# Performance work log

Hardware: AMD Instinct MI355X
Metric: run time of the kernel (lower is better)

The kernel has to match this reference:

```python
import jax, jax.numpy as jnp
import numpy as np

B, T = 16, 64
IN, H = 256, 512          # input_size, hidden_size (= output_size)
M, W, R = 256, 64, 4      # nr_cells, cell_size, read_heads
NN_IN = R * W + IN        # controller input size = 512
IFACE = R * W + 3 * W + 5 * R + 3  # 471
DELTA = 1e-6


def _lin(key, fan_out, fan_in):
    k1, k2 = jax.random.split(key)
    s = 1.0 / np.sqrt(fan_in)
    Wm = jax.random.uniform(k1, (fan_out, fan_in), minval=-s, maxval=s, dtype=jnp.float32)
    b = jax.random.uniform(k2, (fan_out,), minval=-s, maxval=s, dtype=jnp.float32)
    return Wm, b


def setup_inputs() -> dict:
    key = jax.random.key(0)
    ks = jax.random.split(key, 8)
    x = jax.random.normal(ks[0], (B, T, IN), dtype=jnp.float32)
    Wih0, bih0 = _lin(ks[1], 4 * H, NN_IN)
    Whh0, bhh0 = _lin(ks[2], 4 * H, H)
    Wih1, bih1 = _lin(ks[3], 4 * H, H)
    Whh1, bhh1 = _lin(ks[4], 4 * H, H)
    Wout, bout = _lin(ks[5], H, H)              # output_weights
    Wif, bif = _lin(ks[6], IFACE, H)            # memory interface_weights
    Wmem, bmem = _lin(ks[7], IN, R * W + H)     # mem_out
    return dict(x=x, Wih0=Wih0, bih0=bih0, Whh0=Whh0, bhh0=bhh0,
                Wih1=Wih1, bih1=bih1, Whh1=Whh1, bhh1=bhh1,
                Wout=Wout, bout=bout, Wif=Wif, bif=bif, Wmem=Wmem, bmem=bmem)


def _lstm(x, h, c, Wih, bih, Whh, bhh):
    g = x @ Wih.T + bih + h @ Whh.T + bhh
    i, f, gg, o = jnp.split(g, 4, axis=-1)  # torch LSTMCell gate order i,f,g,o
    i, f, o = jax.nn.sigmoid(i), jax.nn.sigmoid(f), jax.nn.sigmoid(o)
    c = f * c + i * jnp.tanh(gg)
    return o * jnp.tanh(c), c


def _content_weights(mem, keys, strengths):
    # mem (B,M,W), keys (B,K,W), strengths (B,K) -> softmax cosine weights (B,K,M)
    mn = mem / (jnp.linalg.norm(mem, axis=2, keepdims=True) + DELTA)
    kn = keys / (jnp.linalg.norm(keys, axis=2, keepdims=True) + DELTA)
    sim = jnp.einsum('bkw,bmw->bkm', kn, mn)
    return jax.nn.softmax(sim * strengths[:, :, None], axis=2)


def _dnc_forward(x, Wih0, bih0, Whh0, bhh0, Wih1, bih1, Whh1, bhh1,
                 Wout, bout, Wif, bif, Wmem, bmem):
    Bz, Tz = x.shape[0], x.shape[1]
    eye_mask = 1.0 - jnp.eye(M, dtype=x.dtype)
    # NOTE: in the source, last_read (zeros at init) is concatenated to EVERY
    # timestep's input and never updated inside the layer time loop.
    last_read = jnp.zeros((Bz, Tz, R * W), dtype=x.dtype)
    xs = jnp.swapaxes(jnp.concatenate([x, last_read], axis=-1), 0, 1)  # (T,B,NN_IN)

    def step(carry, xt):
        h0, c0, h1, c1, mem, link, prec, rw, ww, usage = carry
        h0, c0 = _lstm(xt, h0, c0, Wih0, bih0, Whh0, bhh0)
        h1, c1 = _lstm(h0, h1, c1, Wih1, bih1, Whh1, bhh1)
        out = h1 @ Wout.T + bout
        xi = h1 @ Wif.T + bif  # (B, IFACE)
        o1 = R * W
        rk = jnp.tanh(xi[:, :o1]).reshape(Bz, R, W)
        rs = jax.nn.softplus(xi[:, o1:o1 + R])
        o2 = o1 + R
        wk = jnp.tanh(xi[:, o2:o2 + W]).reshape(Bz, 1, W)
        ws = jax.nn.softplus(xi[:, o2 + W:o2 + W + 1])          # (B,1)
        ev = jax.nn.sigmoid(xi[:, o2 + W + 1:o2 + 2 * W + 1])   # erase (B,W)
        wv = jnp.tanh(xi[:, o2 + 2 * W + 1:o2 + 3 * W + 1])     # write vec (B,W)
        o3 = o2 + 3 * W + 1
        fg = jax.nn.sigmoid(xi[:, o3:o3 + R])                   # free gates (B,R)
        ag = jax.nn.sigmoid(xi[:, o3 + R:o3 + R + 1])           # alloc gate (B,1)
        wg = jax.nn.sigmoid(xi[:, o3 + R + 1:o3 + R + 2])       # write gate (B,1)
        rm = jax.nn.softmax(xi[:, o3 + R + 2:].reshape(Bz, R, 3), axis=-1)
        # --- usage update (single write head: 1 - prod(1-ww) == ww) ---
        usage = usage + (1.0 - usage) * ww
        psi = jnp.prod(1.0 - fg[:, :, None] * rw, axis=1)
        usage = usage * psi
        # --- write content weighting ---
        wcw = _content_weights(mem, wk, ws)[:, 0]  # (B,M)
        # --- allocation via sort + exclusive cumprod + inverse scatter ---
        u = DELTA + (1.0 - DELTA) * usage
        idx = jnp.argsort(u, axis=1)  # ascending usage = free list
        su = jnp.take_along_axis(u, idx, axis=1)
        prod_excl = jnp.cumprod(jnp.concatenate([jnp.ones((Bz, 1), u.dtype), su], 1), axis=1)[:, :-1]
        sa = (1.0 - su) * prod_excl
        alloc = jnp.take_along_axis(sa, jnp.argsort(idx, axis=1), axis=1)  # (B,M)
        # --- write weighting ---
        ww = wg * (ag * alloc + (1.0 - ag) * wcw)  # (B,M)
        # --- memory erase + write ---
        mem = mem * (1.0 - ww[:, :, None] * ev[:, None, :]) + ww[:, :, None] * wv[:, None, :]
        # --- temporal link matrix (diag zeroed) + precedence ---
        link = (1.0 - ww[:, :, None] - ww[:, None, :]) * link + ww[:, :, None] * prec[:, None, :]
        link = link * eye_mask
        prec = (1.0 - jnp.sum(ww, axis=1, keepdims=True)) * prec + ww
        # --- read: content + forward/backward directional modes ---
        cw = _content_weights(mem, rk, rs)            # (B,R,M)
        fwd = jnp.einsum('bmn,brn->brm', link, rw)    # L @ rw_prev
        bwd = jnp.einsum('brm,bmn->brn', rw, link)    # rw_prev @ L
        rw = rm[:, :, 0:1] * bwd + rm[:, :, 1:2] * fwd + rm[:, :, 2:3] * cw
        read_vecs = jnp.einsum('brm,bmw->brw', rw, mem).reshape(Bz, R * W)
        y = jnp.concatenate([out, read_vecs], axis=1) @ Wmem.T + bmem  # mem_out, dropout=0
        return (h0, c0, h1, c1, mem, link, prec, rw, ww, usage), y

    z = lambda *s: jnp.zeros(s, dtype=x.dtype)
    init = (z(Bz, H), z(Bz, H), z(Bz, H), z(Bz, H),
            z(Bz, M, W), z(Bz, M, M), z(Bz, M), z(Bz, R, M), z(Bz, M), z(Bz, M))
    _, ys = jax.lax.scan(step, init, xs)
    return jnp.swapaxes(ys, 0, 1)  # (B,T,IN)


def reference(x, Wih0, bih0, Whh0, bhh0, Wih1, bih1, Whh1, bhh1,
              Wout, bout, Wif, bif, Wmem, bmem):
    return _dnc_forward(x, Wih0, bih0, Whh0, bhh0, Wih1, bih1, Whh1, bhh1,
                        Wout, bout, Wif, bif, Wmem, bmem)
```

## Files before the change

### kernel.cpp

```cpp
#include <hip/hip_runtime.h>
#include <math.h>


#define BZ    16
#define TZ    64
#define HID   512
#define NCELL 256
#define CSZ   64
#define NRD   4
#define G4H   2048
#define IFC   471
#define DEL   1e-6f
#define SMT   257

__device__ __forceinline__ float sig_(float x) { return 1.f / (1.f + expf(-x)); }
__device__ __forceinline__ float splus_(float x) { return fmaxf(x, 0.f) + log1pf(expf(-fabsf(x))); }

__global__ __launch_bounds__(256) void k_transpose(const float* __restrict__ src,
                                                   float* __restrict__ dst,
                                                   int rows, int cols, int kmax, int dst_stride) {
  __shared__ float tile[32][33];
  int c0 = blockIdx.x * 32, r0 = blockIdx.y * 32;
  int tx = threadIdx.x, ty = threadIdx.y;
  for (int i = ty; i < 32; i += 8) {
    int r = r0 + i, c = c0 + tx;
    tile[i][tx] = (r < rows && c < cols) ? src[(size_t)r * cols + c] : 0.f;
  }
  __syncthreads();
  for (int i = ty; i < 32; i += 8) {
    int c = c0 + i, r = r0 + tx;
    if (c < kmax && r < rows) dst[(size_t)c * dst_stride + r] = tile[tx][i];
  }
}

__global__ __launch_bounds__(256) void k_xpart(const float* __restrict__ x,
                                               const float* __restrict__ Wih0T,
                                               const float* __restrict__ bih0,
                                               const float* __restrict__ bhh0,
                                               float* __restrict__ xpart) {
  const int lane = threadIdx.x, ty = threadIdx.y;
  const int jg = blockIdx.x * 64 + lane;
  const int tb0 = blockIdx.y * 16;
  __shared__ float sx[16][256];
  const int tid = ty * 64 + lane;
  for (int idx = tid; idx < 16 * 256; idx += 256) {
    int row = idx >> 8, k = idx & 255;
    int tb = tb0 + row, tt = tb >> 4, bb = tb & 15;
    sx[row][k] = x[((size_t)bb * TZ + tt) * 256 + k];
  }
  __syncthreads();
  float acc[4] = {0.f, 0.f, 0.f, 0.f};
  for (int k = 0; k < 256; ++k) {
    float wv = Wih0T[(size_t)k * G4H + jg];
#pragma unroll
    for (int i = 0; i < 4; ++i) acc[i] = fmaf(wv, sx[ty * 4 + i][k], acc[i]);
  }
  float bias = bih0[jg] + bhh0[jg];
#pragma unroll
  for (int i = 0; i < 4; ++i)
    xpart[(size_t)(tb0 + ty * 4 + i) * G4H + jg] = acc[i] + bias;
}

__global__ __launch_bounds__(256) void k_lstm_step(
    const float* __restrict__ xpart,
    const float* __restrict__ Whh0T,
    const float* __restrict__ Wih1T, const float* __restrict__ Whh1T,
    const float* __restrict__ bih1, const float* __restrict__ bhh1,
    float* __restrict__ h0, float* __restrict__ c0,
    float* __restrict__ h1, float* __restrict__ c1,
    float* __restrict__ h1_all, int ph) {
  const int jl = threadIdx.x, ks = threadIdx.y;
  const int tid = ks * 64 + jl;
  const int bid = blockIdx.x;
  const int grp = bid >> 7;
  const int lb = bid & 127;
  const int b = lb >> 3, jb = lb & 7;
  const int j = jb * 64 + jl;
  __shared__ float sh0[512], sh1[512];
  __shared__ float sred[4][4][64];

  if (grp == 0) {
    if (ph >= TZ) return;
    const int t = ph, po = t & 1, pn = po ^ 1;
    const float* h0o = h0 + ((size_t)po * BZ + b) * HID;
    for (int k = tid; k < 512; k += 256) sh0[k] = h0o[k];
    __syncthreads();
    float a0 = 0.f, a1 = 0.f, a2 = 0.f, a3 = 0.f;
    const int kb = ks * 128;
#pragma unroll 8
    for (int k = kb; k < kb + 128; ++k) {
      const float hk = sh0[k];
      const float* wr = Whh0T + (size_t)k * G4H + j;
      a0 = fmaf(hk, wr[0], a0);
      a1 = fmaf(hk, wr[512], a1);
      a2 = fmaf(hk, wr[1024], a2);
      a3 = fmaf(hk, wr[1536], a3);
    }
    sred[ks][0][jl] = a0; sred[ks][1][jl] = a1; sred[ks][2][jl] = a2; sred[ks][3][jl] = a3;
    __syncthreads();
    if (ks == 0) {
      const float* xp = xpart + ((size_t)t * BZ + b) * G4H;
      float gi = sred[0][0][jl] + sred[1][0][jl] + sred[2][0][jl] + sred[3][0][jl] + xp[j];
      float gf = sred[0][1][jl] + sred[1][1][jl] + sred[2][1][jl] + sred[3][1][jl] + xp[512 + j];
      float gg = sred[0][2][jl] + sred[1][2][jl] + sred[2][2][jl] + sred[3][2][jl] + xp[1024 + j];
      float go_ = sred[0][3][jl] + sred[1][3][jl] + sred[2][3][jl] + sred[3][3][jl] + xp[1536 + j];
      gi = sig_(gi); gf = sig_(gf); go_ = sig_(go_); gg = tanhf(gg);
      float* cp = c0 + b * HID + j;
      float cc = gf * (*cp) + gi * gg;
      *cp = cc;
      h0[((size_t)pn * BZ + b) * HID + j] = go_ * tanhf(cc);
    }
  } else {
    if (ph < 1) return;
    const int t = ph - 1, po = t & 1, pn = po ^ 1;
    const float* h0n = h0 + ((size_t)pn * BZ + b) * HID;
    const float* h1o = h1 + ((size_t)po * BZ + b) * HID;
    for (int k = tid; k < 512; k += 256) { sh0[k] = h0n[k]; sh1[k] = h1o[k]; }
    __syncthreads();
    float a0 = 0.f, a1 = 0.f, a2 = 0.f, a3 = 0.f;
    const int kb = ks * 128;
#pragma unroll 4
    for (int k = kb; k < kb + 128; ++k) {
      const float x0 = sh0[k], x1 = sh1[k];
      const float* wi = Wih1T + (size_t)k * G4H + j;
      const float* wh = Whh1T + (size_t)k * G4H + j;
      a0 = fmaf(x0, wi[0], fmaf(x1, wh[0], a0));
      a1 = fmaf(x0, wi[512], fmaf(x1, wh[512], a1));
      a2 = fmaf(x0, wi[1024], fmaf(x1, wh[1024], a2));
      a3 = fmaf(x0, wi[1536], fmaf(x1, wh[1536], a3));
    }
    sred[ks][0][jl] = a0; sred[ks][1][jl] = a1; sred[ks][2][jl] = a2; sred[ks][3][jl] = a3;
    __syncthreads();
    if (ks == 0) {
      float gi = sred[0][0][jl] + sred[1][0][jl] + sred[2][0][jl] + sred[3][0][jl] + bih1[j] + bhh1[j];
      float gf = sred[0][1][jl] + sred[1][1][jl] + sred[2][1][jl] + sred[3][1][jl] + bih1[512 + j] + bhh1[512 + j];
      float gg = sred[0][2][jl] + sred[1][2][jl] + sred[2][2][jl] + sred[3][2][jl] + bih1[1024 + j] + bhh1[1024 + j];
      float go_ = sred[0][3][jl] + sred[1][3][jl] + sred[2][3][jl] + sred[3][3][jl] + bih1[1536 + j] + bhh1[1536 + j];
      gi = sig_(gi); gf = sig_(gf); go_ = sig_(go_); gg = tanhf(gg);
      float* cp = c1 + b * HID + j;
      float cc = gf * (*cp) + gi * gg;
      *cp = cc;
      float hv = go_ * tanhf(cc);
      h1[((size_t)pn * BZ + b) * HID + j] = hv;
      h1_all[((size_t)t * BZ + b) * HID + j] = hv;
    }
  }
}

__global__ __launch_bounds__(256) void k_xiout(const float* __restrict__ h1_all,
                                               const float* __restrict__ WoutT,
                                               const float* __restrict__ WifT,
                                               const float* __restrict__ bout,
                                               const float* __restrict__ bif,
                                               float* __restrict__ out_all,
                                               float* __restrict__ xi_all) {
  const int lane = threadIdx.x, ty = threadIdx.y;
  const int u = blockIdx.x * 64 + lane;
  const int row0 = blockIdx.y * 16;
  __shared__ float sh[16][512];
  const int tid = ty * 64 + lane;
  for (int idx = tid; idx < 16 * 512; idx += 256) {
    int r2 = idx >> 9, k = idx & 511;
    sh[r2][k] = h1_all[(size_t)(row0 + r2) * 512 + k];
  }
  __syncthreads();
  const bool isout = (u < 512);
  int uc = isout ? u : (u - 512);
  if (!isout && uc >= IFC) uc = 0;
  const float* wcol = isout ? (WoutT + u) : (WifT + uc);
  float bias = isout ? bout[u] : ((u - 512) < IFC ? bif[u - 512] : 0.f);
  float acc[4] = {0.f, 0.f, 0.f, 0.f};
  for (int k = 0; k < 512; ++k) {
    float wv = wcol[(size_t)k * 512];
#pragma unroll
    for (int i = 0; i < 4; ++i) acc[i] = fmaf(wv, sh[ty * 4 + i][k], acc[i]);
  }
#pragma unroll
  for (int i = 0; i < 4; ++i) {
    int row = row0 + ty * 4 + i;
    if (isout) out_all[(size_t)row * 512 + u] = acc[i] + bias;
    else if ((u - 512) < IFC) xi_all[(size_t)row * 512 + (u - 512)] = acc[i] + bias;
  }
}

__global__ __launch_bounds__(1024, 1) void k_memchain(const float* __restrict__ xi_all,
                                                      float* __restrict__ linkg,
                                                      float* __restrict__ rv_all) {
  const int b = blockIdx.x;
  const int tid = threadIdx.x;
  const int lane = tid & 63;
  const int wv = tid >> 6;
  const int m8 = tid & 255;
  const int seg = tid >> 8;
  float* LNK = linkg + (size_t)b * (NCELL * NCELL);

  __shared__ __align__(16) float smemT[CSZ * SMT];
  __shared__ __align__(16) float sxi[472];
  __shared__ __align__(16) float srkn[NRD][64];
  __shared__ __align__(16) float swkn[64];
  __shared__ __align__(16) float sev[64];
  __shared__ __align__(16) float swvv[64];
  __shared__ __align__(16) float sscal[40];
  __shared__ __align__(16) float srw[NRD][256];
  __shared__ __align__(16) float sww[256];
  __shared__ __align__(16) float susage[256];
  __shared__ __align__(16) float sprec[256];
  __shared__ __align__(16) float ssim[NRD][256];
  __shared__ __align__(16) float sfwd[NRD][256];
  __shared__ __align__(16) float sbwd[NRD][264];
  __shared__ __align__(16) float sa[256];
  __shared__ __align__(16) float sc_[256];
  __shared__ float sb_[256];
  __shared__ int srank[256];
  __shared__ __align__(16) float scr[4][5 * 264];
  __shared__ float sred2[64];

  for (int i = tid; i < CSZ * SMT; i += 1024) smemT[i] = 0.f;
  if (tid < 256) {
    sww[tid] = 0.f; susage[tid] = 0.f; sprec[tid] = 0.f;
    srw[0][tid] = 0.f; srw[1][tid] = 0.f; srw[2][tid] = 0.f; srw[3][tid] = 0.f;
  }
  for (int i = tid; i < (NCELL * NCELL) / 4; i += 1024)
    ((float4*)LNK)[i] = make_float4(0.f, 0.f, 0.f, 0.f);
  __syncthreads();

  for (int t = 0; t < TZ; ++t) {
    if (tid < IFC) sxi[tid] = xi_all[((size_t)t * BZ + b) * 512 + tid];
    __syncthreads();
    if (wv < 4) {
      float v = tanhf(sxi[wv * 64 + lane]);
      float s2 = v * v;
#pragma unroll
      for (int off = 32; off; off >>= 1) s2 += __shfl_xor(s2, off);
      srkn[wv][lane] = v / (sqrtf(s2) + DEL);
    } else if (wv == 4) {
      float v = tanhf(sxi[260 + lane]);
      float s2 = v * v;
#pragma unroll
      for (int off = 32; off; off >>= 1) s2 += __shfl_xor(s2, off);
      swkn[lane] = v / (sqrtf(s2) + DEL);
    } else if (wv == 5) {
      sev[lane] = sig_(sxi[325 + lane]);
    } else if (wv == 6) {
      swvv[lane] = tanhf(sxi[389 + lane]);
    } else if (wv == 7) {
      if (lane < 4) sscal[lane] = splus_(sxi[256 + lane]);
      if (lane == 4) sscal[4] = splus_(sxi[324]);
      if (lane >= 8 && lane < 12) sscal[lane] = sig_(sxi[453 + (lane - 8)]);
      if (lane == 12) sscal[12] = sig_(sxi[457]);
      if (lane == 13) sscal[13] = sig_(sxi[458]);
      if (lane >= 16 && lane < 20) {
        int r = lane - 16;
        float a = sxi[459 + r * 3], b2 = sxi[460 + r * 3], c2 = sxi[461 + r * 3];
        float mx3 = fmaxf(a, fmaxf(b2, c2));
        float ea = expf(a - mx3), eb = expf(b2 - mx3), ec = expf(c2 - mx3);
        float iv = 1.f / (ea + eb + ec);
        sscal[20 + r * 3 + 0] = ea * iv;
        sscal[20 + r * 3 + 1] = eb * iv;
        sscal[20 + r * 3 + 2] = ec * iv;
      }
    }
    __syncthreads();

    float un_r = 0.f;
    if (tid < 256) {
      float wwo = sww[tid], uo = susage[tid];
      float u1 = uo + (1.f - uo) * wwo;
      float psi = 1.f;
#pragma unroll
      for (int r = 0; r < 4; ++r) psi *= 1.f - sscal[8 + r] * srw[r][tid];
      un_r = u1 * psi;
      susage[tid] = un_r;
    }
    {
      float dot = 0.f, nn = 0.f;
#pragma unroll 4
      for (int w = seg * 16; w < seg * 16 + 16; ++w) {
        float mv = smemT[w * SMT + m8];
        dot = fmaf(mv, swkn[w], dot);
        nn = fmaf(mv, mv, nn);
      }
      scr[seg][0 * 264 + m8] = dot;
      scr[seg][1 * 264 + m8] = nn;
    }
    __syncthreads();
    float e_r = 0.f, simv = 0.f;
    if (tid < 256) {
      float dot = scr[0][tid] + scr[1][tid] + scr[2][tid] + scr[3][tid];
      float nn = scr[0][264 + tid] + scr[1][264 + tid] + scr[2][264 + tid] + scr[3][264 + tid];
      simv = sscal[4] * dot / (sqrtf(nn) + DEL);
      float mx = simv;
#pragma unroll
      for (int off = 32; off; off >>= 1) mx = fmaxf(mx, __shfl_xor(mx, off));
      if (lane == 0) sred2[wv] = mx;
    }
    __syncthreads();
    if (tid < 256) {
      float mx = fmaxf(fmaxf(sred2[0], sred2[1]), fmaxf(sred2[2], sred2[3]));
      e_r = expf(simv - mx);
      float s = e_r;
#pragma unroll
      for (int off = 32; off; off >>= 1) s += __shfl_xor(s, off);
      if (lane == 0) sred2[8 + wv] = s;
    }
    __syncthreads();
    float wcw_r = 0.f;
    if (tid < 256) {
      float sm = sred2[8] + sred2[9] + sred2[10] + sred2[11];
      wcw_r = e_r / sm;
      sa[tid] = DEL + (1.f - DEL) * un_r;
    }
    __syncthreads();

    {
      float um = sa[m8];
      int cnt = 0;
      for (int j2 = seg * 64; j2 < seg * 64 + 64; ++j2) {
        float uj = sa[j2];
        cnt += (uj < um || (uj == um && j2 < m8)) ? 1 : 0;
      }
      ((int*)scr[seg])[m8] = cnt;
    }
    __syncthreads();
    if (tid < 256) {
      int rank = ((int*)scr[0])[tid] + ((int*)scr[1])[tid] + ((int*)scr[2])[tid] + ((int*)scr[3])[tid];
      srank[tid] = rank;
      sb_[rank] = sa[tid];
    }
    __syncthreads();
    float inc = 0.f;
    if (tid < 256) {
      inc = sb_[tid];
#pragma unroll
      for (int off = 1; off < 64; off <<= 1) {
        float pp = __shfl_up(inc, off);
        if (lane >= off) inc *= pp;
      }
      if (lane == 63) sred2[16 + wv] = inc;
    }
    __syncthreads();
    if (tid < 256) {
      float pref = 1.f;
      for (int w2 = 0; w2 < wv; ++w2) pref *= sred2[16 + w2];
      float excl = __shfl_up(inc, 1);
      if (lane == 0) excl = 1.f;
      sc_[tid] = excl * pref;
    }
    __syncthreads();

    if (tid < 256) {
      float alo = (1.f - sa[tid]) * sc_[srank[tid]];
      float wwn = sscal[13] * (sscal[12] * alo + (1.f - sscal[12]) * wcw_r);
      sww[tid] = wwn;
      float s = wwn;
#pragma unroll
      for (int off = 32; off; off >>= 1) s += __shfl_xor(s, off);
      if (lane == 0) sred2[24 + wv] = s;
    }
    __syncthreads();
    if (tid == 0) sscal[14] = sred2[24] + sred2[25] + sred2[26] + sred2[27];

    {
      float wm = sww[m8];
      float nn = 0.f, d0 = 0.f, d1 = 0.f, d2 = 0.f, d3 = 0.f;
#pragma unroll 4
      for (int w = seg * 16; w < seg * 16 + 16; ++w) {
        float v = smemT[w * SMT + m8];
        v = v * (1.f - wm * sev[w]) + wm * swvv[w];
        smemT[w * SMT + m8] = v;
        nn = fmaf(v, v, nn);
        d0 = fmaf(v, srkn[0][w], d0);
        d1 = fmaf(v, srkn[1][w], d1);
        d2 = fmaf(v, srkn[2][w], d2);
        d3 = fmaf(v, srkn[3][w], d3);
      }
      scr[seg][0 * 264 + m8] = nn;
      scr[seg][1 * 264 + m8] = d0;
      scr[seg][2 * 264 + m8] = d1;
      scr[seg][3 * 264 + m8] = d2;
      scr[seg][4 * 264 + m8] = d3;
    }
    for (int i = tid; i < NRD * 264; i += 1024) ((float*)sbwd)[i] = 0.f;
    __syncthreads();
    float sv0 = 0.f, sv1 = 0.f, sv2 = 0.f, sv3 = 0.f;
    float e0 = 0.f, e1 = 0.f, e2 = 0.f, e3 = 0.f;
    if (tid < 256) {
      float nn = scr[0][tid] + scr[1][tid] + scr[2][tid] + scr[3][tid];
      float invn = 1.f / (sqrtf(nn) + DEL);
      sv0 = sscal[0] * (scr[0][264 + tid] + scr[1][264 + tid] + scr[2][264 + tid] + scr[3][264 + tid]) * invn;
      sv1 = sscal[1] * (scr[0][528 + tid] + scr[1][528 + tid] + scr[2][528 + tid] + scr[3][528 + tid]) * invn;
      sv2 = sscal[2] * (scr[0][792 + tid] + scr[1][792 + tid] + scr[2][792 + tid] + scr[3][792 + tid]) * invn;
      sv3 = sscal[3] * (scr[0][1056 + tid] + scr[1][1056 + tid] + scr[2][1056 + tid] + scr[3][1056 + tid]) * invn;
      float m0 = sv0, m1 = sv1, m2 = sv2, m3 = sv3;
#pragma unroll
      for (int off = 32; off; off >>= 1) {
        m0 = fmaxf(m0, __shfl_xor(m0, off));
        m1 = fmaxf(m1, __shfl_xor(m1, off));
        m2 = fmaxf(m2, __shfl_xor(m2, off));
        m3 = fmaxf(m3, __shfl_xor(m3, off));
      }
      if (lane == 0) {
        sred2[wv * 4 + 0] = m0; sred2[wv * 4 + 1] = m1;
        sred2[wv * 4 + 2] = m2; sred2[wv * 4 + 3] = m3;
      }
    }
    __syncthreads();
    if (tid < 256) {
      float m0 = fmaxf(fmaxf(sred2[0], sred2[4]), fmaxf(sred2[8], sred2[12]));
      float m1 = fmaxf(fmaxf(sred2[1], sred2[5]), fmaxf(sred2[9], sred2[13]));
      float m2 = fmaxf(fmaxf(sred2[2], sred2[6]), fmaxf(sred2[10], sred2[14]));
      float m3 = fmaxf(fmaxf(sred2[3], sred2[7]), fmaxf(sred2[11], sred2[15]));
      e0 = expf(sv0 - m0); e1 = expf(sv1 - m1); e2 = expf(sv2 - m2); e3 = expf(sv3 - m3);
      float s0 = e0, s1 = e1, s2 = e2, s3 = e3;
#pragma unroll
      for (int off = 32; off; off >>= 1) {
        s0 += __shfl_xor(s0, off); s1 += __shfl_xor(s1, off);
        s2 += __shfl_xor(s2, off); s3 += __shfl_xor(s3, off);
      }
      if (lane == 0) {
        sred2[32 + wv * 4 + 0] = s0; sred2[32 + wv * 4 + 1] = s1;
        sred2[32 + wv * 4 + 2] = s2; sred2[32 + wv * 4 + 3] = s3;
      }
    }
    __syncthreads();
    if (tid < 256) {
      float s0 = sred2[32] + sred2[36] + sred2[40] + sred2[44];
      float s1 = sred2[33] + sred2[37] + sred2[41] + sred2[45];
      float s2 = sred2[34] + sred2[38] + sred2[42] + sred2[46];
      float s3 = sred2[35] + sred2[39] + sred2[43] + sred2[47];
      ssim[0][tid] = e0 / s0; ssim[1][tid] = e1 / s1;
      ssim[2][tid] = e2 / s2; ssim[3][tid] = e3 / s3;
    }

    {
      const float4 r0 = ((const float4*)srw[0])[lane];
      const float4 r1 = ((const float4*)srw[1])[lane];
      const float4 r2 = ((const float4*)srw[2])[lane];
      const float4 r3 = ((const float4*)srw[3])[lane];
      const float4 wc = ((const float4*)sww)[lane];
      const float4 pc = ((const float4*)sprec)[lane];
      const int n0 = lane * 4;
      float4 bp0 = make_float4(0.f, 0.f, 0.f, 0.f);
      float4 bp1 = make_float4(0.f, 0.f, 0.f, 0.f);
      float4 bp2 = make_float4(0.f, 0.f, 0.f, 0.f);
      float4 bp3 = make_float4(0.f, 0.f, 0.f, 0.f);
      for (int rr = 0; rr < 16; ++rr) {
        const int m = wv * 16 + rr;
        const float wm = sww[m];
        float4 lv = ((float4*)(LNK + (size_t)m * 256))[lane];
        lv.x = (1.f - wm - wc.x) * lv.x + wm * pc.x;
        lv.y = (1.f - wm - wc.y) * lv.y + wm * pc.y;
        lv.z = (1.f - wm - wc.z) * lv.z + wm * pc.z;
        lv.w = (1.f - wm - wc.w) * lv.w + wm * pc.w;
        if (m == n0 + 0) lv.x = 0.f;
        if (m == n0 + 1) lv.y = 0.f;
        if (m == n0 + 2) lv.z = 0.f;
        if (m == n0 + 3) lv.w = 0.f;
        ((float4*)(LNK + (size_t)m * 256))[lane] = lv;
        float f0 = lv.x * r0.x + lv.y * r0.y + lv.z * r0.z + lv.w * r0.w;
        float f1 = lv.x * r1.x + lv.y * r1.y + lv.z * r1.z + lv.w * r1.w;
        float f2 = lv.x * r2.x + lv.y * r2.y + lv.z * r2.z + lv.w * r2.w;
        float f3 = lv.x * r3.x + lv.y * r3.y + lv.z * r3.z + lv.w * r3.w;
#pragma unroll
        for (int off = 32; off; off >>= 1) {
          f0 += __shfl_xor(f0, off); f1 += __shfl_xor(f1, off);
          f2 += __shfl_xor(f2, off); f3 += __shfl_xor(f3, off);
        }
        if (lane == 0) {
          sfwd[0][m] = f0; sfwd[1][m] = f1; sfwd[2][m] = f2; sfwd[3][m] = f3;
        }
        const float s0 = srw[0][m], s1 = srw[1][m], s2 = srw[2][m], s3 = srw[3][m];
        bp0.x = fmaf(lv.x, s0, bp0.x); bp0.y = fmaf(lv.y, s0, bp0.y);
        bp0.z = fmaf(lv.z, s0, bp0.z); bp0.w = fmaf(lv.w, s0, bp0.w);
        bp1.x = fmaf(lv.x, s1, bp1.x); bp1.y = fmaf(lv.y, s1, bp1.y);
        bp1.z = fmaf(lv.z, s1, bp1.z); bp1.w = fmaf(lv.w, s1, bp1.w);
        bp2.x = fmaf(lv.x, s2, bp2.x); bp2.y = fmaf(lv.y, s2, bp2.y);
        bp2.z = fmaf(lv.z, s2, bp2.z); bp2.w = fmaf(lv.w, s2, bp2.w);
        bp3.x = fmaf(lv.x, s3, bp3.x); bp3.y = fmaf(lv.y, s3, bp3.y);
        bp3.z = fmaf(lv.z, s3, bp3.z); bp3.w = fmaf(lv.w, s3, bp3.w);
      }
      atomicAdd(&sbwd[0][n0 + 0], bp0.x); atomicAdd(&sbwd[0][n0 + 1], bp0.y);
      atomicAdd(&sbwd[0][n0 + 2], bp0.z); atomicAdd(&sbwd[0][n0 + 3], bp0.w);
      atomicAdd(&sbwd[1][n0 + 0], bp1.x); atomicAdd(&sbwd[1][n0 + 1], bp1.y);
      atomicAdd(&sbwd[1][n0 + 2], bp1.z); atomicAdd(&sbwd[1][n0 + 3], bp1.w);
      atomicAdd(&sbwd[2][n0 + 0], bp2.x); atomicAdd(&sbwd[2][n0 + 1], bp2.y);
      atomicAdd(&sbwd[2][n0 + 2], bp2.z); atomicAdd(&sbwd[2][n0 + 3], bp2.w);
      atomicAdd(&sbwd[3][n0 + 0], bp3.x); atomicAdd(&sbwd[3][n0 + 1], bp3.y);
      atomicAdd(&sbwd[3][n0 + 2], bp3.z); atomicAdd(&sbwd[3][n0 + 3], bp3.w);
    }
    __syncthreads();

    if (tid < 256) {
#pragma unroll
      for (int r = 0; r < 4; ++r) {
        float rwn = sscal[20 + r * 3 + 0] * sbwd[r][tid] +
                    sscal[20 + r * 3 + 1] * sfwd[r][tid] +
                    sscal[20 + r * 3 + 2] * ssim[r][tid];
        srw[r][tid] = rwn;
      }
      sprec[tid] = (1.f - sscal[14]) * sprec[tid] + sww[tid];
    }
    __syncthreads();

    {
      const int r = tid >> 8, sg = (tid >> 6) & 3, w = lane;
      float acc = 0.f;
#pragma unroll 4
      for (int m2 = sg * 64; m2 < sg * 64 + 64; ++m2)
        acc = fmaf(srw[r][m2], smemT[w * SMT + m2], acc);
      scr[sg][r * 64 + w] = acc;
    }
    __syncthreads();
    if (tid < 256)
      rv_all[((size_t)t * BZ + b) * 256 + tid] =
          scr[0][tid] + scr[1][tid] + scr[2][tid] + scr[3][tid];
    __syncthreads();
  }
}

__global__ __launch_bounds__(256) void k_y(const float* __restrict__ out_all,
                                           const float* __restrict__ rv_all,
                                           const float* __restrict__ WmemT,
                                           const float* __restrict__ bmem,
                                           float* __restrict__ y) {
  const int lane = threadIdx.x, ty = threadIdx.y;
  const int o = blockIdx.x * 64 + lane;
  const int tb0 = blockIdx.y * 16;
  __shared__ float sin_[16][768];
  const int tid = ty * 64 + lane;
  for (int idx = tid; idx < 16 * 768; idx += 256) {
    int row = idx / 768, k = idx % 768;
    int tb = tb0 + row;
    sin_[row][k] = (k < 512) ? out_all[(size_t)tb * HID + k]
                             : rv_all[(size_t)tb * 256 + (k - 512)];
  }
  __syncthreads();
  float acc[4] = {0.f, 0.f, 0.f, 0.f};
  for (int k = 0; k < 768; ++k) {
    float wv = WmemT[(size_t)k * 256 + o];
#pragma unroll
    for (int i = 0; i < 4; ++i) acc[i] = fmaf(wv, sin_[ty * 4 + i][k], acc[i]);
  }
  float bo = bmem[o];
#pragma unroll
  for (int i = 0; i < 4; ++i) {
    int tb = tb0 + ty * 4 + i;
    int tt = tb >> 4, bb = tb & 15;
    y[((size_t)bb * TZ + tt) * 256 + o] = acc[i] + bo;
  }
}

extern "C" void kernel_launch(void* const* d_in, const int* in_sizes, int n_in,
                              void* d_out, int out_size, void* d_ws, size_t ws_size,
                              hipStream_t stream) {
  (void)in_sizes; (void)n_in; (void)out_size; (void)ws_size;
  const float* x    = (const float*)d_in[0];
  const float* Wih0 = (const float*)d_in[1];
  const float* bih0 = (const float*)d_in[2];
  const float* Whh0 = (const float*)d_in[3];
  const float* bhh0 = (const float*)d_in[4];
  const float* Wih1 = (const float*)d_in[5];
  const float* bih1 = (const float*)d_in[6];
  const float* Whh1 = (const float*)d_in[7];
  const float* bhh1 = (const float*)d_in[8];
  const float* Wout = (const float*)d_in[9];
  const float* bout = (const float*)d_in[10];
  const float* Wif  = (const float*)d_in[11];
  const float* bif  = (const float*)d_in[12];
  const float* Wmem = (const float*)d_in[13];
  const float* bmem = (const float*)d_in[14];
  float* y = (float*)d_out;

  float* p = (float*)d_ws;
  auto take = [&](size_t n) { float* q = p; p += n; return q; };
  float* Wih0T   = take((size_t)256 * 2048);
  float* Whh0T   = take((size_t)512 * 2048);
  float* Wih1T   = take((size_t)512 * 2048);
  float* Whh1T   = take((size_t)512 * 2048);
  float* WoutT   = take((size_t)512 * 512);
  float* WifT    = take((size_t)512 * 512);
  float* WmemT   = take((size_t)768 * 256);
  float* xpart   = take((size_t)TZ * BZ * G4H);
  float* h1_all  = take((size_t)TZ * BZ * HID);
  float* out_all = take((size_t)TZ * BZ * HID);
  float* xi_all  = take((size_t)TZ * BZ * 512);
  float* rv_all  = take((size_t)TZ * BZ * 256);
  float* linkg   = take((size_t)BZ * NCELL * NCELL);
  float* zstart  = p;
  float* h0      = take((size_t)2 * BZ * HID);
  float* c0      = take((size_t)BZ * HID);
  float* h1      = take((size_t)2 * BZ * HID);
  float* c1      = take((size_t)BZ * HID);
  size_t zbytes = (size_t)((char*)p - (char*)zstart);

  hipMemsetAsync(zstart, 0, zbytes, stream);

  dim3 tb32(32, 8);
  hipLaunchKernelGGL(k_transpose, dim3(8, 64), tb32, 0, stream, Wih0, Wih0T, 2048, 512, 256, 2048);
  hipLaunchKernelGGL(k_transpose, dim3(16, 64), tb32, 0, stream, Whh0, Whh0T, 2048, 512, 512, 2048);
  hipLaunchKernelGGL(k_transpose, dim3(16, 64), tb32, 0, stream, Wih1, Wih1T, 2048, 512, 512, 2048);
  hipLaunchKernelGGL(k_transpose, dim3(16, 64), tb32, 0, stream, Whh1, Whh1T, 2048, 512, 512, 2048);
  hipLaunchKernelGGL(k_transpose, dim3(16, 16), tb32, 0, stream, Wout, WoutT, 512, 512, 512, 512);
  hipLaunchKernelGGL(k_transpose, dim3(16, 15), tb32, 0, stream, Wif, WifT, 471, 512, 512, 512);
  hipLaunchKernelGGL(k_transpose, dim3(24, 8), tb32, 0, stream, Wmem, WmemT, 256, 768, 768, 256);

  hipLaunchKernelGGL(k_xpart, dim3(32, 64), dim3(64, 4), 0, stream, x, Wih0T, bih0, bhh0, xpart);

  for (int ph = 0; ph <= TZ; ++ph)
    hipLaunchKernelGGL(k_lstm_step, dim3(256), dim3(64, 4), 0, stream,
                       xpart, Whh0T, Wih1T, Whh1T, bih1, bhh1,
                       h0, c0, h1, c1, h1_all, ph);

  hipLaunchKernelGGL(k_xiout, dim3(16, 64), dim3(64, 4), 0, stream,
                     h1_all, WoutT, WifT, bout, bif, out_all, xi_all);

  hipLaunchKernelGGL(k_memchain, dim3(16), dim3(1024), 0, stream,
                     xi_all, linkg, rv_all);

  hipLaunchKernelGGL(k_y, dim3(4, 64), dim3(64, 4), 0, stream, out_all, rv_all, WmemT, bmem, y);
}
```

Before: 4.559 ms.

## Replace per-step LSTM launches with persistent kernel, LDS-resident weights, grid barrier

Replaces 65 separate LSTM step launches with one persistent kernel of 192 blocks. Each block keeps its slice of the recurrent weights in shared memory and the steps are separated by an atomic grid barrier. This removes per-step launch overhead and repeated global weight reads, and drops three weight transposes. The memory-chain kernel also gets vectorised rank counting, software-prefetched link rows and a float4 read-vector loop with padded SMT. The grid barrier assumes all 192 blocks are co-resident, and the large LDS footprint limits each CU to one block.

```diff
diff --git a/kernel.cpp b/kernel.cpp
--- a/kernel.cpp
+++ b/kernel.cpp
@@ -11,7 +11,8 @@
 #define G4H   2048
 #define IFC   471
 #define DEL   1e-6f
-#define SMT   257
+#define SMT   260
+#define NBLK  192
 
 __device__ __forceinline__ float sig_(float x) { return 1.f / (1.f + expf(-x)); }
 __device__ __forceinline__ float splus_(float x) { return fmaxf(x, 0.f) + log1pf(expf(-fabsf(x))); }
@@ -61,88 +62,204 @@
     xpart[(size_t)(tb0 + ty * 4 + i) * G4H + jg] = acc[i] + bias;
 }
 
-__global__ __launch_bounds__(256) void k_lstm_step(
+__device__ __forceinline__ void gbar(unsigned* cnt, int ph, int tid) {
+  __syncthreads();
+  if (tid == 0) {
+    __hip_atomic_fetch_add(&cnt[ph], 1u, __ATOMIC_RELEASE, __HIP_MEMORY_SCOPE_AGENT);
+    while (__hip_atomic_load(&cnt[ph], __ATOMIC_ACQUIRE, __HIP_MEMORY_SCOPE_AGENT) < NBLK)
+      __builtin_amdgcn_s_sleep(2);
+  }
+  __syncthreads();
+}
+
+__global__ __launch_bounds__(256, 1) void k_lstm_persist(
     const float* __restrict__ xpart,
-    const float* __restrict__ Whh0T,
-    const float* __restrict__ Wih1T, const float* __restrict__ Whh1T,
+    const float* __restrict__ Whh0,
+    const float* __restrict__ Wih1, const float* __restrict__ Whh1,
     const float* __restrict__ bih1, const float* __restrict__ bhh1,
-    float* __restrict__ h0, float* __restrict__ c0,
-    float* __restrict__ h1, float* __restrict__ c1,
-    float* __restrict__ h1_all, int ph) {
-  const int jl = threadIdx.x, ks = threadIdx.y;
-  const int tid = ks * 64 + jl;
+    float* __restrict__ h0g, float* __restrict__ h1g,
+    float* __restrict__ h1_all, unsigned* __restrict__ cnt) {
+  const int tid = threadIdx.x;
   const int bid = blockIdx.x;
-  const int grp = bid >> 7;
-  const int lb = bid & 127;
-  const int b = lb >> 3, jb = lb & 7;
-  const int j = jb * 64 + jl;
-  __shared__ float sh0[512], sh1[512];
-  __shared__ float sred[4][4][64];
-
-  if (grp == 0) {
-    if (ph >= TZ) return;
-    const int t = ph, po = t & 1, pn = po ^ 1;
-    const float* h0o = h0 + ((size_t)po * BZ + b) * HID;
-    for (int k = tid; k < 512; k += 256) sh0[k] = h0o[k];
-    __syncthreads();
-    float a0 = 0.f, a1 = 0.f, a2 = 0.f, a3 = 0.f;
-    const int kb = ks * 128;
-#pragma unroll 8
-    for (int k = kb; k < kb + 128; ++k) {
-      const float hk = sh0[k];
-      const float* wr = Whh0T + (size_t)k * G4H + j;
-      a0 = fmaf(hk, wr[0], a0);
-      a1 = fmaf(hk, wr[512], a1);
-      a2 = fmaf(hk, wr[1024], a2);
-      a3 = fmaf(hk, wr[1536], a3);
-    }
-    sred[ks][0][jl] = a0; sred[ks][1][jl] = a1; sred[ks][2][jl] = a2; sred[ks][3][jl] = a3;
-    __syncthreads();
-    if (ks == 0) {
-      const float* xp = xpart + ((size_t)t * BZ + b) * G4H;
-      float gi = sred[0][0][jl] + sred[1][0][jl] + sred[2][0][jl] + sred[3][0][jl] + xp[j];
-      float gf = sred[0][1][jl] + sred[1][1][jl] + sred[2][1][jl] + sred[3][1][jl] + xp[512 + j];
-      float gg = sred[0][2][jl] + sred[1][2][jl] + sred[2][2][jl] + sred[3][2][jl] + xp[1024 + j];
-      float go_ = sred[0][3][jl] + sred[1][3][jl] + sred[2][3][jl] + sred[3][3][jl] + xp[1536 + j];
-      gi = sig_(gi); gf = sig_(gf); go_ = sig_(go_); gg = tanhf(gg);
-      float* cp = c0 + b * HID + j;
-      float cc = gf * (*cp) + gi * gg;
-      *cp = cc;
-      h0[((size_t)pn * BZ + b) * HID + j] = go_ * tanhf(cc);
+  __shared__ float S[37264];
+
+  if (bid < 64) {
+    float* w0 = S;
+    float* hl = S + 16768;
+    float* sc = hl + 8320;
+    float* xpl = sc + 4096;
+    float* c0l = xpl + 512;
+    const int j0 = bid * 8;
+    for (int lr = 0; lr < 32; ++lr) {
+      int g = lr >> 3, jj = lr & 7;
+      const float* src = Whh0 + (size_t)(g * 512 + j0 + jj) * 512;
+      for (int k = tid; k < 512; k += 256) w0[lr * 524 + k] = src[k];
+    }
+    for (int i = tid; i < 128; i += 256) c0l[i] = 0.f;
+    const int ks = tid & 7, bq = (tid >> 3) & 3, jj = tid >> 5;
+    const int wr0 = (0 * 8 + jj) * 524, wr1 = (1 * 8 + jj) * 524,
+              wr2 = (2 * 8 + jj) * 524, wr3 = (3 * 8 + jj) * 524;
+    const int hb0 = (bq * 4 + 0) * 520, hb1 = (bq * 4 + 1) * 520,
+              hb2 = (bq * 4 + 2) * 520, hb3 = (bq * 4 + 3) * 520;
+    for (int ph = 0; ph < 65; ++ph) {
+      if (ph < 64) {
+        const int t = ph, po = t & 1, pn = po ^ 1;
+        for (int q = tid; q < 2048; q += 256) {
+          int b = q >> 7, kq = q & 127;
+          ((float4*)&hl[b * 520])[kq] = ((const float4*)&h0g[(size_t)(po * 16 + b) * 512])[kq];
+        }
+        {
+          int b = tid >> 5, g = (tid >> 3) & 3, j2 = tid & 7;
+          xpl[tid] = xpart[((size_t)t * 16 + b) * G4H + g * 512 + j0 + j2];
+          int t2 = tid + 256;
+          b = t2 >> 5; g = (t2 >> 3) & 3; j2 = t2 & 7;
+          xpl[t2] = xpart[((size_t)t * 16 + b) * G4H + g * 512 + j0 + j2];
+        }
+        __syncthreads();
+        float4 a0 = {0,0,0,0}, a1 = {0,0,0,0}, a2 = {0,0,0,0}, a3 = {0,0,0,0};
+#pragma unroll 4
+        for (int i = 0; i < 16; ++i) {
+          const int off = ks * 4 + 32 * i;
+          float4 w4a = *(const float4*)&w0[wr0 + off];
+          float4 w4b = *(const float4*)&w0[wr1 + off];
+          float4 w4c = *(const float4*)&w0[wr2 + off];
+          float4 w4d = *(const float4*)&w0[wr3 + off];
+          float4 h4a = *(const float4*)&hl[hb0 + off];
+          float4 h4b = *(const float4*)&hl[hb1 + off];
+          float4 h4c = *(const float4*)&hl[hb2 + off];
+          float4 h4d = *(const float4*)&hl[hb3 + off];
+          a0.x += w4a.x*h4a.x + w4a.y*h4a.y + w4a.z*h4a.z + w4a.w*h4a.w;
+          a0.y += w4a.x*h4b.x + w4a.y*h4b.y + w4a.z*h4b.z + w4a.w*h4b.w;
+          a0.z += w4a.x*h4c.x + w4a.y*h4c.y + w4a.z*h4c.z + w4a.w*h4c.w;
+          a0.w += w4a.x*h4d.x + w4a.y*h4d.y + w4a.z*h4d.z + w4a.w*h4d.w;
+          a1.x += w4b.x*h4a.x + w4b.y*h4a.y + w4b.z*h4a.z + w4b.w*h4a.w;
+          a1.y += w4b.x*h4b.x + w4b.y*h4b.y + w4b.z*h4b.z + w4b.w*h4b.w;
+          a1.z += w4b.x*h4c.x + w4b.y*h4c.y + w4b.z*h4c.z + w4b.w*h4c.w;
+          a1.w += w4b.x*h4d.x + w4b.y*h4d.y + w4b.z*h4d.z + w4b.w*h4d.w;
+          a2.x += w4c.x*h4a.x + w4c.y*h4a.y + w4c.z*h4a.z + w4c.w*h4a.w;
+          a2.y += w4c.x*h4b.x + w4c.y*h4b.y + w4c.z*h4b.z + w4c.w*h4b.w;
+          a2.z += w4c.x*h4c.x + w4c.y*h4c.y + w4c.z*h4c.z + w4c.w*h4c.w;
+          a2.w += w4c.x*h4d.x + w4c.y*h4d.y + w4c.z*h4d.z + w4c.w*h4d.w;
+          a3.x += w4d.x*h4a.x + w4d.y*h4a.y + w4d.z*h4a.z + w4d.w*h4a.w;
+          a3.y += w4d.x*h4b.x + w4d.y*h4b.y + w4d.z*h4b.z + w4d.w*h4b.w;
+          a3.z += w4d.x*h4c.x + w4d.y*h4c.y + w4d.z*h4c.z + w4d.w*h4c.w;
+          a3.w += w4d.x*h4d.x + w4d.y*h4d.y + w4d.z*h4d.z + w4d.w*h4d.w;
+        }
+        *(float4*)&sc[ks * 512 + (0 * 8 + jj) * 16 + bq * 4] = a0;
+        *(float4*)&sc[ks * 512 + (1 * 8 + jj) * 16 + bq * 4] = a1;
+        *(float4*)&sc[ks * 512 + (2 * 8 + jj) * 16 + bq * 4] = a2;
+        *(float4*)&sc[ks * 512 + (3 * 8 + jj) * 16 + bq * 4] = a3;
+        __syncthreads();
+        if (tid < 128) {
+          const int b = tid >> 3, j2 = tid & 7;
+          float gs[4];
+#pragma unroll
+          for (int g = 0; g < 4; ++g) {
+            float s = 0.f;
+#pragma unroll
+            for (int k2 = 0; k2 < 8; ++k2) s += sc[k2 * 512 + (g * 8 + j2) * 16 + b];
+            gs[g] = s + xpl[b * 32 + g * 8 + j2];
+          }
+          float gi = sig_(gs[0]), gf = sig_(gs[1]), gg = tanhf(gs[2]), go = sig_(gs[3]);
+          float cc = gf * c0l[j2 * 16 + b] + gi * gg;
+          c0l[j2 * 16 + b] = cc;
+          h0g[(size_t)(pn * 16 + b) * 512 + j0 + j2] = go * tanhf(cc);
+        }
+      }
+      gbar(cnt, ph, tid);
     }
   } else {
-    if (ph < 1) return;
-    const int t = ph - 1, po = t & 1, pn = po ^ 1;
-    const float* h0n = h0 + ((size_t)pn * BZ + b) * HID;
-    const float* h1o = h1 + ((size_t)po * BZ + b) * HID;
-    for (int k = tid; k < 512; k += 256) { sh0[k] = h0n[k]; sh1[k] = h1o[k]; }
-    __syncthreads();
-    float a0 = 0.f, a1 = 0.f, a2 = 0.f, a3 = 0.f;
-    const int kb = ks * 128;
+    float* w1 = S;
+    float* h0l = S + 16448;
+    float* h1l = h0l + 8320;
+    float* sc = h1l + 8320;
+    float* c1l = sc + 4096;
+    float* bl = c1l + 64;
+    const int b1 = bid - 64;
+    const int j0 = b1 * 4;
+    for (int lr = 0; lr < 16; ++lr) {
+      int g = lr >> 2, jj = lr & 3;
+      const float* si = Wih1 + (size_t)(g * 512 + j0 + jj) * 512;
+      const float* sh = Whh1 + (size_t)(g * 512 + j0 + jj) * 512;
+      for (int k = tid; k < 512; k += 256) {
+        w1[lr * 1028 + k] = si[k];
+        w1[lr * 1028 + 512 + k] = sh[k];
+      }
+    }
+    if (tid < 64) c1l[tid] = 0.f;
+    if (tid < 16) {
+      int g = tid >> 2, jj = tid & 3;
+      bl[tid] = bih1[g * 512 + j0 + jj] + bhh1[g * 512 + j0 + jj];
+    }
+    const int ks = tid & 15, bq = (tid >> 4) & 3, jj = tid >> 6;
+    const int wr0 = (0 * 4 + jj) * 1028, wr1 = (1 * 4 + jj) * 1028,
+              wr2 = (2 * 4 + jj) * 1028, wr3 = (3 * 4 + jj) * 1028;
+    const int hb0 = (bq * 4 + 0) * 520, hb1 = (bq * 4 + 1) * 520,
+              hb2 = (bq * 4 + 2) * 520, hb3 = (bq * 4 + 3) * 520;
+    for (int ph = 0; ph < 65; ++ph) {
+      if (ph >= 1) {
+        const int t = ph - 1, po = t & 1, pn = po ^ 1;
+        for (int q = tid; q < 2048; q += 256) {
+          int b = q >> 7, kq = q & 127;
+          ((float4*)&h0l[b * 520])[kq] = ((const float4*)&h0g[(size_t)(pn * 16 + b) * 512])[kq];
+          ((float4*)&h1l[b * 520])[kq] = ((const float4*)&h1g[(size_t)(po * 16 + b) * 512])[kq];
+        }
+        __syncthreads();
+        float4 a0 = {0,0,0,0}, a1 = {0,0,0,0}, a2 = {0,0,0,0}, a3 = {0,0,0,0};
 #pragma unroll 4
-    for (int k = kb; k < kb + 128; ++k) {
-      const float x0 = sh0[k], x1 = sh1[k];
-      const float* wi = Wih1T + (size_t)k * G4H + j;
-      const float* wh = Whh1T + (size_t)k * G4H + j;
-      a0 = fmaf(x0, wi[0], fmaf(x1, wh[0], a0));
-      a1 = fmaf(x0, wi[512], fmaf(x1, wh[512], a1));
-      a2 = fmaf(x0, wi[1024], fmaf(x1, wh[1024], a2));
-      a3 = fmaf(x0, wi[1536], fmaf(x1, wh[1536], a3));
-    }
-    sred[ks][0][jl] = a0; sred[ks][1][jl] = a1; sred[ks][2][jl] = a2; sred[ks][3][jl] = a3;
-    __syncthreads();
-    if (ks == 0) {
-      float gi = sred[0][0][jl] + sred[1][0][jl] + sred[2][0][jl] + sred[3][0][jl] + bih1[j] + bhh1[j];
-      float gf = sred[0][1][jl] + sred[1][1][jl] + sred[2][1][jl] + sred[3][1][jl] + bih1[512 + j] + bhh1[512 + j];
-      float gg = sred[0][2][jl] + sred[1][2][jl] + sred[2][2][jl] + sred[3][2][jl] + bih1[1024 + j] + bhh1[1024 + j];
-      float go_ = sred[0][3][jl] + sred[1][3][jl] + sred[2][3][jl] + sred[3][3][jl] + bih1[1536 + j] + bhh1[1536 + j];
-      gi = sig_(gi); gf = sig_(gf); go_ = sig_(go_); gg = tanhf(gg);
-      float* cp = c1 + b * HID + j;
-      float cc = gf * (*cp) + gi * gg;
-      *cp = cc;
-      float hv = go_ * tanhf(cc);
-      h1[((size_t)pn * BZ + b) * HID + j] = hv;
-      h1_all[((size_t)t * BZ + b) * HID + j] = hv;
+        for (int i = 0; i < 16; ++i) {
+          const int offw = ks * 4 + 64 * i;
+          const int offh = (i < 8) ? offw : (offw - 512);
+          const float* hsrc = (i < 8) ? h0l : h1l;
+          float4 w4a = *(const float4*)&w1[wr0 + offw];
+          float4 w4b = *(const float4*)&w1[wr1 + offw];
+          float4 w4c = *(const float4*)&w1[wr2 + offw];
+          float4 w4d = *(const float4*)&w1[wr3 + offw];
+          float4 h4a = *(const float4*)&hsrc[hb0 + offh];
+          float4 h4b = *(const float4*)&hsrc[hb1 + offh];
+          float4 h4c = *(const float4*)&hsrc[hb2 + offh];
+          float4 h4d = *(const float4*)&hsrc[hb3 + offh];
+          a0.x += w4a.x*h4a.x + w4a.y*h4a.y + w4a.z*h4a.z + w4a.w*h4a.w;
+          a0.y += w4a.x*h4b.x + w4a.y*h4b.y + w4a.z*h4b.z + w4a.w*h4b.w;
+          a0.z += w4a.x*h4c.x + w4a.y*h4c.y + w4a.z*h4c.z + w4a.w*h4c.w;
+          a0.w += w4a.x*h4d.x + w4a.y*h4d.y + w4a.z*h4d.z + w4a.w*h4d.w;
+          a1.x += w4b.x*h4a.x + w4b.y*h4a.y + w4b.z*h4a.z + w4b.w*h4a.w;
+          a1.y += w4b.x*h4b.x + w4b.y*h4b.y + w4b.z*h4b.z + w4b.w*h4b.w;
+          a1.z += w4b.x*h4c.x + w4b.y*h4c.y + w4b.z*h4c.z + w4b.w*h4c.w;
+          a1.w += w4b.x*h4d.x + w4b.y*h4d.y + w4b.z*h4d.z + w4b.w*h4d.w;
+          a2.x += w4c.x*h4a.x + w4c.y*h4a.y + w4c.z*h4a.z + w4c.w*h4a.w;
+          a2.y += w4c.x*h4b.x + w4c.y*h4b.y + w4c.z*h4b.z + w4c.w*h4b.w;
+          a2.z += w4c.x*h4c.x + w4c.y*h4c.y + w4c.z*h4c.z + w4c.w*h4c.w;
+          a2.w += w4c.x*h4d.x + w4c.y*h4d.y + w4c.z*h4d.z + w4c.w*h4d.w;
+          a3.x += w4d.x*h4a.x + w4d.y*h4a.y + w4d.z*h4a.z + w4d.w*h4a.w;
+          a3.y += w4d.x*h4b.x + w4d.y*h4b.y + w4d.z*h4b.z + w4d.w*h4b.w;
+          a3.z += w4d.x*h4c.x + w4d.y*h4c.y + w4d.z*h4c.z + w4d.w*h4c.w;
+          a3.w += w4d.x*h4d.x + w4d.y*h4d.y + w4d.z*h4d.z + w4d.w*h4d.w;
+        }
+        *(float4*)&sc[ks * 256 + (0 * 4 + jj) * 16 + bq * 4] = a0;
+        *(float4*)&sc[ks * 256 + (1 * 4 + jj) * 16 + bq * 4] = a1;
+        *(float4*)&sc[ks * 256 + (2 * 4 + jj) * 16 + bq * 4] = a2;
+        *(float4*)&sc[ks * 256 + (3 * 4 + jj) * 16 + bq * 4] = a3;
+        __syncthreads();
+        if (tid < 64) {
+          const int b = tid >> 2, j2 = tid & 3;
+          float gs[4];
+#pragma unroll
+          for (int g = 0; g < 4; ++g) {
+            float s = 0.f;
+#pragma unroll
+            for (int k2 = 0; k2 < 16; ++k2) s += sc[k2 * 256 + (g * 4 + j2) * 16 + b];
+            gs[g] = s + bl[g * 4 + j2];
+          }
+          float gi = sig_(gs[0]), gf = sig_(gs[1]), gg = tanhf(gs[2]), go = sig_(gs[3]);
+          float cc = gf * c1l[j2 * 16 + b] + gi * gg;
+          c1l[j2 * 16 + b] = cc;
+          float hv = go * tanhf(cc);
+          h1g[(size_t)(pn * 16 + b) * 512 + j0 + j2] = hv;
+          h1_all[((size_t)t * 16 + b) * 512 + j0 + j2] = hv;
+        }
+      }
+      gbar(cnt, ph, tid);
     }
   }
 }
@@ -314,12 +431,17 @@
 
     {
       float um = sa[m8];
-      int cnt = 0;
-      for (int j2 = seg * 64; j2 < seg * 64 + 64; ++j2) {
-        float uj = sa[j2];
-        cnt += (uj < um || (uj == um && j2 < m8)) ? 1 : 0;
-      }
-      ((int*)scr[seg])[m8] = cnt;
+      int cnt2 = 0;
+#pragma unroll
+      for (int c4 = 0; c4 < 16; ++c4) {
+        float4 uq = ((const float4*)&sa[seg * 64])[c4];
+        int j2 = seg * 64 + c4 * 4;
+        cnt2 += (uq.x < um || (uq.x == um && (j2 + 0) < m8)) ? 1 : 0;
+        cnt2 += (uq.y < um || (uq.y == um && (j2 + 1) < m8)) ? 1 : 0;
+        cnt2 += (uq.z < um || (uq.z == um && (j2 + 2) < m8)) ? 1 : 0;
+        cnt2 += (uq.w < um || (uq.w == um && (j2 + 3) < m8)) ? 1 : 0;
+      }
+      ((int*)scr[seg])[m8] = cnt2;
     }
     __syncthreads();
     if (tid < 256) {
@@ -440,44 +562,58 @@
       const float4 wc = ((const float4*)sww)[lane];
       const float4 pc = ((const float4*)sprec)[lane];
       const int n0 = lane * 4;
-      float4 bp0 = make_float4(0.f, 0.f, 0.f, 0.f);
-      float4 bp1 = make_float4(0.f, 0.f, 0.f, 0.f);
-      float4 bp2 = make_float4(0.f, 0.f, 0.f, 0.f);
-      float4 bp3 = make_float4(0.f, 0.f, 0.f, 0.f);
-      for (int rr = 0; rr < 16; ++rr) {
-        const int m = wv * 16 + rr;
-        const float wm = sww[m];
-        float4 lv = ((float4*)(LNK + (size_t)m * 256))[lane];
-        lv.x = (1.f - wm - wc.x) * lv.x + wm * pc.x;
-        lv.y = (1.f - wm - wc.y) * lv.y + wm * pc.y;
-        lv.z = (1.f - wm - wc.z) * lv.z + wm * pc.z;
-        lv.w = (1.f - wm - wc.w) * lv.w + wm * pc.w;
-        if (m == n0 + 0) lv.x = 0.f;
-        if (m == n0 + 1) lv.y = 0.f;
-        if (m == n0 + 2) lv.z = 0.f;
-        if (m == n0 + 3) lv.w = 0.f;
-        ((float4*)(LNK + (size_t)m * 256))[lane] = lv;
-        float f0 = lv.x * r0.x + lv.y * r0.y + lv.z * r0.z + lv.w * r0.w;
-        float f1 = lv.x * r1.x + lv.y * r1.y + lv.z * r1.z + lv.w * r1.w;
-        float f2 = lv.x * r2.x + lv.y * r2.y + lv.z * r2.z + lv.w * r2.w;
-        float f3 = lv.x * r3.x + lv.y * r3.y + lv.z * r3.z + lv.w * r3.w;
-#pragma unroll
-        for (int off = 32; off; off >>= 1) {
-          f0 += __shfl_xor(f0, off); f1 += __shfl_xor(f1, off);
-          f2 += __shfl_xor(f2, off); f3 += __shfl_xor(f3, off);
-        }
-        if (lane == 0) {
-          sfwd[0][m] = f0; sfwd[1][m] = f1; sfwd[2][m] = f2; sfwd[3][m] = f3;
-        }
-        const float s0 = srw[0][m], s1 = srw[1][m], s2 = srw[2][m], s3 = srw[3][m];
-        bp0.x = fmaf(lv.x, s0, bp0.x); bp0.y = fmaf(lv.y, s0, bp0.y);
-        bp0.z = fmaf(lv.z, s0, bp0.z); bp0.w = fmaf(lv.w, s0, bp0.w);
-        bp1.x = fmaf(lv.x, s1, bp1.x); bp1.y = fmaf(lv.y, s1, bp1.y);
-        bp1.z = fmaf(lv.z, s1, bp1.z); bp1.w = fmaf(lv.w, s1, bp1.w);
-        bp2.x = fmaf(lv.x, s2, bp2.x); bp2.y = fmaf(lv.y, s2, bp2.y);
-        bp2.z = fmaf(lv.z, s2, bp2.z); bp2.w = fmaf(lv.w, s2, bp2.w);
-        bp3.x = fmaf(lv.x, s3, bp3.x); bp3.y = fmaf(lv.y, s3, bp3.y);
-        bp3.z = fmaf(lv.z, s3, bp3.z); bp3.w = fmaf(lv.w, s3, bp3.w);
+      const int rbase = wv * 16;
+      float4* LW = (float4*)LNK;
+      float4 bp0 = {0,0,0,0}, bp1 = {0,0,0,0}, bp2 = {0,0,0,0}, bp3 = {0,0,0,0};
+      float4 nxa = LW[(rbase + 0) * 64 + lane];
+      float4 nxb = LW[(rbase + 1) * 64 + lane];
+      float4 nxc = LW[(rbase + 2) * 64 + lane];
+      float4 nxd = LW[(rbase + 3) * 64 + lane];
+#pragma unroll
+      for (int rq = 0; rq < 4; ++rq) {
+        float4 ca = nxa, cb = nxb, cg = nxc, cd = nxd;
+        if (rq < 3) {
+          nxa = LW[(rbase + rq * 4 + 4) * 64 + lane];
+          nxb = LW[(rbase + rq * 4 + 5) * 64 + lane];
+          nxc = LW[(rbase + rq * 4 + 6) * 64 + lane];
+          nxd = LW[(rbase + rq * 4 + 7) * 64 + lane];
+        }
+#pragma unroll
+        for (int rj = 0; rj < 4; ++rj) {
+          const int m = rbase + rq * 4 + rj;
+          float4 lv = (rj == 0) ? ca : (rj == 1) ? cb : (rj == 2) ? cg : cd;
+          const float wm = sww[m];
+          lv.x = (1.f - wm - wc.x) * lv.x + wm * pc.x;
+          lv.y = (1.f - wm - wc.y) * lv.y + wm * pc.y;
+          lv.z = (1.f - wm - wc.z) * lv.z + wm * pc.z;
+          lv.w = (1.f - wm - wc.w) * lv.w + wm * pc.w;
+          if (m == n0 + 0) lv.x = 0.f;
+          if (m == n0 + 1) lv.y = 0.f;
+          if (m == n0 + 2) lv.z = 0.f;
+          if (m == n0 + 3) lv.w = 0.f;
+          LW[m * 64 + lane] = lv;
+          float f0 = lv.x * r0.x + lv.y * r0.y + lv.z * r0.z + lv.w * r0.w;
+          float f1 = lv.x * r1.x + lv.y * r1.y + lv.z * r1.z + lv.w * r1.w;
+          float f2 = lv.x * r2.x + lv.y * r2.y + lv.z * r2.z + lv.w * r2.w;
+          float f3 = lv.x * r3.x + lv.y * r3.y + lv.z * r3.z + lv.w * r3.w;
+#pragma unroll
+          for (int off = 32; off; off >>= 1) {
+            f0 += __shfl_xor(f0, off); f1 += __shfl_xor(f1, off);
+            f2 += __shfl_xor(f2, off); f3 += __shfl_xor(f3, off);
+          }
+          if (lane == 0) {
+            sfwd[0][m] = f0; sfwd[1][m] = f1; sfwd[2][m] = f2; sfwd[3][m] = f3;
+          }
+          const float s0 = srw[0][m], s1 = srw[1][m], s2 = srw[2][m], s3 = srw[3][m];
+          bp0.x = fmaf(lv.x, s0, bp0.x); bp0.y = fmaf(lv.y, s0, bp0.y);
+          bp0.z = fmaf(lv.z, s0, bp0.z); bp0.w = fmaf(lv.w, s0, bp0.w);
+          bp1.x = fmaf(lv.x, s1, bp1.x); bp1.y = fmaf(lv.y, s1, bp1.y);
+          bp1.z = fmaf(lv.z, s1, bp1.z); bp1.w = fmaf(lv.w, s1, bp1.w);
+          bp2.x = fmaf(lv.x, s2, bp2.x); bp2.y = fmaf(lv.y, s2, bp2.y);
+          bp2.z = fmaf(lv.z, s2, bp2.z); bp2.w = fmaf(lv.w, s2, bp2.w);
+          bp3.x = fmaf(lv.x, s3, bp3.x); bp3.y = fmaf(lv.y, s3, bp3.y);
+          bp3.z = fmaf(lv.z, s3, bp3.z); bp3.w = fmaf(lv.w, s3, bp3.w);
+        }
       }
       atomicAdd(&sbwd[0][n0 + 0], bp0.x); atomicAdd(&sbwd[0][n0 + 1], bp0.y);
       atomicAdd(&sbwd[0][n0 + 2], bp0.z); atomicAdd(&sbwd[0][n0 + 3], bp0.w);
@@ -506,8 +642,11 @@
       const int r = tid >> 8, sg = (tid >> 6) & 3, w = lane;
       float acc = 0.f;
 #pragma unroll 4
-      for (int m2 = sg * 64; m2 < sg * 64 + 64; ++m2)
-        acc = fmaf(srw[r][m2], smemT[w * SMT + m2], acc);
+      for (int mq = sg * 16; mq < sg * 16 + 16; ++mq) {
+        float4 rq = ((const float4*)srw[r])[mq];
+        float4 mv = *(const float4*)&smemT[w * SMT + mq * 4];
+        acc += rq.x * mv.x + rq.y * mv.y + rq.z * mv.z + rq.w * mv.w;
+      }
       scr[sg][r * 64 + w] = acc;
     }
     __syncthreads();
@@ -574,9 +713,6 @@
   float* p = (float*)d_ws;
   auto take = [&](size_t n) { float* q = p; p += n; return q; };
   float* Wih0T   = take((size_t)256 * 2048);
-  float* Whh0T   = take((size_t)512 * 2048);
-  float* Wih1T   = take((size_t)512 * 2048);
-  float* Whh1T   = take((size_t)512 * 2048);
   float* WoutT   = take((size_t)512 * 512);
   float* WifT    = take((size_t)512 * 512);
   float* WmemT   = take((size_t)768 * 256);
@@ -587,29 +723,24 @@
   float* rv_all  = take((size_t)TZ * BZ * 256);
   float* linkg   = take((size_t)BZ * NCELL * NCELL);
   float* zstart  = p;
-  float* h0      = take((size_t)2 * BZ * HID);
-  float* c0      = take((size_t)BZ * HID);
-  float* h1      = take((size_t)2 * BZ * HID);
-  float* c1      = take((size_t)BZ * HID);
+  float* h0g     = take((size_t)2 * BZ * HID);
+  float* h1g     = take((size_t)2 * BZ * HID);
+  float* cntf    = take((size_t)128);
   size_t zbytes = (size_t)((char*)p - (char*)zstart);
+  unsigned* cnt = (unsigned*)cntf;
 
   hipMemsetAsync(zstart, 0, zbytes, stream);
 
   dim3 tb32(32, 8);
   hipLaunchKernelGGL(k_transpose, dim3(8, 64), tb32, 0, stream, Wih0, Wih0T, 2048, 512, 256, 2048);
-  hipLaunchKernelGGL(k_transpose, dim3(16, 64), tb32, 0, stream, Whh0, Whh0T, 2048, 512, 512, 2048);
-  hipLaunchKernelGGL(k_transpose, dim3(16, 64), tb32, 0, stream, Wih1, Wih1T, 2048, 512, 512, 2048);
-  hipLaunchKernelGGL(k_transpose, dim3(16, 64), tb32, 0, stream, Whh1, Whh1T, 2048, 512, 512, 2048);
   hipLaunchKernelGGL(k_transpose, dim3(16, 16), tb32, 0, stream, Wout, WoutT, 512, 512, 512, 512);
   hipLaunchKernelGGL(k_transpose, dim3(16, 15), tb32, 0, stream, Wif, WifT, 471, 512, 512, 512);
   hipLaunchKernelGGL(k_transpose, dim3(24, 8), tb32, 0, stream, Wmem, WmemT, 256, 768, 768, 256);
 
   hipLaunchKernelGGL(k_xpart, dim3(32, 64), dim3(64, 4), 0, stream, x, Wih0T, bih0, bhh0, xpart);
 
-  for (int ph = 0; ph <= TZ; ++ph)
-    hipLaunchKernelGGL(k_lstm_step, dim3(256), dim3(64, 4), 0, stream,
-                       xpart, Whh0T, Wih1T, Whh1T, bih1, bhh1,
-                       h0, c0, h1, c1, h1_all, ph);
+  hipLaunchKernelGGL(k_lstm_persist, dim3(NBLK), dim3(256), 0, stream,
+                     xpart, Whh0, Wih1, Whh1, bih1, bhh1, h0g, h1g, h1_all, cnt);
 
   hipLaunchKernelGGL(k_xiout, dim3(16, 64), dim3(64, 4), 0, stream,
                      h1_all, WoutT, WifT, bout, bif, out_all, xi_all);
```

Result: slower. 5.102 ms (+11.9%).
